# Performance work log

Hardware: AMD Instinct MI355X
Metric: run time of the kernel (lower is better)

Reference implementation:

```python
import jax, jax.numpy as jnp
import numpy as np

V, T, D, H, L, F, B = 50257, 1024, 1024, 16, 10, 4096, 2
HD = D // H  # head_dim = 64
EPS = 1e-5


def sinusoidal_pos(seq_len, d_model):
    pos = np.arange(seq_len)[:, None].astype(np.float32)
    i = np.arange(d_model // 2).astype(np.float32)
    inv = 1.0 / (10000.0 ** (2.0 * i / d_model))
    ang = pos * inv[None, :]
    pe = np.zeros((seq_len, d_model), dtype=np.float32)
    pe[:, 0::2] = np.sin(ang)
    pe[:, 1::2] = np.cos(ang)
    return jnp.asarray(pe)


def setup_inputs() -> dict:
    key = jax.random.key(0)
    ks = jax.random.split(key, 16)
    s = 0.02
    return {
        "x": jax.random.randint(ks[0], (B, T), 0, V),
        "emb": jax.random.normal(ks[1], (V, D), jnp.float32) * s,
        "pos": sinusoidal_pos(T, D),
        "Wq": jax.random.normal(ks[2], (L, D, D), jnp.float32) * s,
        "bq": jnp.zeros((L, D), jnp.float32),
        "Wk": jax.random.normal(ks[3], (L, D, D), jnp.float32) * s,
        "bk": jnp.zeros((L, D), jnp.float32),
        "Wv": jax.random.normal(ks[4], (L, D, D), jnp.float32) * s,
        "bv": jnp.zeros((L, D), jnp.float32),
        "ln_g": jnp.ones((L, D), jnp.float32),
        "ln_b": jnp.zeros((L, D), jnp.float32),
        "W1": jax.random.normal(ks[5], (L, D, F), jnp.float32) * s,
        "b1": jnp.zeros((L, F), jnp.float32),
        "W2": jax.random.normal(ks[6], (L, F, D), jnp.float32) * s,
        "b2": jnp.zeros((L, D), jnp.float32),
        "lnf_g": jnp.ones((D,), jnp.float32),
        "lnf_b": jnp.zeros((D,), jnp.float32),
        "Wout": jax.random.normal(ks[7], (D, V), jnp.float32) * s,
        "bout": jnp.zeros((V,), jnp.float32),
    }


def layer_norm(h, g, b):
    mu = jnp.mean(h, axis=-1, keepdims=True)
    var = jnp.mean(jnp.square(h - mu), axis=-1, keepdims=True)
    return (h - mu) * jax.lax.rsqrt(var + EPS) * g + b


def reference(x, emb, pos, Wq, bq, Wk, bk, Wv, bv, ln_g, ln_b, W1, b1, W2, b2, lnf_g, lnf_b, Wout, bout):
    t = x.shape[1]
    h = emb[x] + pos[None, :t]  # [B,T,D]
    causal = jnp.tril(jnp.ones((t, t), bool))  # True = keep
    scale = 1.0 / jnp.sqrt(jnp.float32(HD))

    def body(h, p):
        wq, bq_, wk, bk_, wv, bv_, g, bln, w1, b1_, w2, b2_ = p
        q = (h @ wq + bq_).reshape(B, t, H, HD)
        k = (h @ wk + bk_).reshape(B, t, H, HD)
        v = (h @ wv + bv_).reshape(B, t, H, HD)
        score = jnp.einsum('bqhd,bkhd->bhqk', q, k) * scale
        score = jnp.where(causal, score, -jnp.inf)
        attn = jax.nn.softmax(score, axis=-1)
        o = jnp.einsum('bhqk,bkhd->bqhd', attn, v).reshape(B, t, D)
        h = layer_norm(h + o, g, bln)
        m = jax.nn.gelu(h @ w1 + b1_, approximate=False) @ w2 + b2_
        h = layer_norm(h + m, g, bln)  # same LayerNorm params reused, as in source
        return h, None

    h, _ = jax.lax.scan(body, h, (Wq, bq, Wk, bk, Wv, bv, ln_g, ln_b, W1, b1, W2, b2))
    h = layer_norm(h, lnf_g, lnf_b)
    return h @ Wout + bout  # [B,T,V]
```

## Files before the change

kernel.cpp:

```cpp
#include <hip/hip_runtime.h>
#include <cstdint>
#include <cstddef>

#define Vv 50257
#define Va 50304
#define Tt 1024
#define Dd 1024
#define Hh 16
#define Ll 10
#define Ff 4096
#define Bb 2
#define Mm (Bb*Tt)
#define KSPLIT 4

typedef float f32x4 __attribute__((ext_vector_type(4)));
typedef __bf16 bf16x8 __attribute__((ext_vector_type(8)));
typedef unsigned short u16x8 __attribute__((ext_vector_type(8)));
typedef unsigned short u16x4 __attribute__((ext_vector_type(4)));

static __device__ __forceinline__ unsigned short f2bf(float f) {
  unsigned int u = __builtin_bit_cast(unsigned int, f);
  unsigned int r = (u + 0x7FFFu + ((u >> 16) & 1u)) >> 16;
  return (unsigned short)r;
}

static __device__ __forceinline__ f32x4 mfma16x16x32(u16x8 a, u16x8 b, f32x4 c) {
  return __builtin_amdgcn_mfma_f32_16x16x32_bf16(
      __builtin_bit_cast(bf16x8, a), __builtin_bit_cast(bf16x8, b), c, 0, 0, 0);
}

static __device__ __forceinline__ void async_cp16(const void* g, void* l) {
  __builtin_amdgcn_global_load_lds(
      (const __attribute__((address_space(1))) unsigned int*)g,
      (__attribute__((address_space(3))) unsigned int*)l, 16, 0, 0);
}

__global__ __launch_bounds__(256) void embed_kernel(
    const int* __restrict__ x, const float* __restrict__ emb,
    const float* __restrict__ pos, float* __restrict__ h,
    unsigned short* __restrict__ hb) {
  int bt = blockIdx.x;
  int t = bt & (Tt - 1);
  int tok = x[bt];
  int i = threadIdx.x * 4;
  f32x4 e = *(const f32x4*)(emb + (size_t)tok * Dd + i);
  f32x4 p = *(const f32x4*)(pos + (size_t)t * Dd + i);
  f32x4 r = e + p;
  *(f32x4*)(h + (size_t)bt * Dd + i) = r;
  u16x4 rb = { f2bf(r[0]), f2bf(r[1]), f2bf(r[2]), f2bf(r[3]) };
  *(u16x4*)(hb + (size_t)bt * Dd + i) = rb;
}

__global__ __launch_bounds__(256) void add_ln_kernel(
    const float* __restrict__ hin, const float* __restrict__ r,
    const float* __restrict__ g, const float* __restrict__ bb,
    float* __restrict__ hout, unsigned short* __restrict__ hbout) {
  int row = blockIdx.x;
  int tid = threadIdx.x;
  size_t off = (size_t)row * Dd + tid * 4;
  f32x4 xv = *(const f32x4*)(hin + off);
  if (r) xv += *(const f32x4*)(r + off);
  float s  = xv[0] + xv[1] + xv[2] + xv[3];
  float ss = xv[0]*xv[0] + xv[1]*xv[1] + xv[2]*xv[2] + xv[3]*xv[3];
  #pragma unroll
  for (int o = 1; o < 64; o <<= 1) {
    s  += __shfl_xor(s, o);
    ss += __shfl_xor(ss, o);
  }
  __shared__ float red[8];
  int wave = tid >> 6, lane = tid & 63;
  if (lane == 0) { red[wave] = s; red[4 + wave] = ss; }
  __syncthreads();
  s  = red[0] + red[1] + red[2] + red[3];
  ss = red[4] + red[5] + red[6] + red[7];
  float mu = s * (1.0f / Dd);
  float var = ss * (1.0f / Dd) - mu * mu;
  float rstd = rsqrtf(var + 1e-5f);
  f32x4 gv = *(const f32x4*)(g + tid * 4);
  f32x4 bv = *(const f32x4*)(bb + tid * 4);
  f32x4 y;
  #pragma unroll
  for (int j = 0; j < 4; ++j) y[j] = (xv[j] - mu) * rstd * gv[j] + bv[j];
  *(f32x4*)(hout + off) = y;
  u16x4 yb = { f2bf(y[0]), f2bf(y[1]), f2bf(y[2]), f2bf(y[3]) };
  *(u16x4*)(hbout + off) = yb;
}

__global__ __launch_bounds__(256) void add_ln_red_kernel(
    const float* __restrict__ hin, const float* __restrict__ parts,
    const float* __restrict__ bias2,
    const float* __restrict__ g, const float* __restrict__ bb,
    float* __restrict__ hout, unsigned short* __restrict__ hbout) {
  int row = blockIdx.x;
  int tid = threadIdx.x;
  size_t off = (size_t)row * Dd + tid * 4;
  f32x4 xv = *(const f32x4*)(hin + off);
  xv += *(const f32x4*)(bias2 + tid * 4);
  #pragma unroll
  for (int s = 0; s < KSPLIT; ++s)
    xv += *(const f32x4*)(parts + (size_t)s * Mm * Dd + off);
  float s  = xv[0] + xv[1] + xv[2] + xv[3];
  float ss = xv[0]*xv[0] + xv[1]*xv[1] + xv[2]*xv[2] + xv[3]*xv[3];
  #pragma unroll
  for (int o = 1; o < 64; o <<= 1) {
    s  += __shfl_xor(s, o);
    ss += __shfl_xor(ss, o);
  }
  __shared__ float red[8];
  int wave = tid >> 6, lane = tid & 63;
  if (lane == 0) { red[wave] = s; red[4 + wave] = ss; }
  __syncthreads();
  s  = red[0] + red[1] + red[2] + red[3];
  ss = red[4] + red[5] + red[6] + red[7];
  float mu = s * (1.0f / Dd);
  float var = ss * (1.0f / Dd) - mu * mu;
  float rstd = rsqrtf(var + 1e-5f);
  f32x4 gv = *(const f32x4*)(g + tid * 4);
  f32x4 bv = *(const f32x4*)(bb + tid * 4);
  f32x4 y;
  #pragma unroll
  for (int j = 0; j < 4; ++j) y[j] = (xv[j] - mu) * rstd * gv[j] + bv[j];
  *(f32x4*)(hout + off) = y;
  u16x4 yb = { f2bf(y[0]), f2bf(y[1]), f2bf(y[2]), f2bf(y[3]) };
  *(u16x4*)(hbout + off) = yb;
}

__global__ __launch_bounds__(256) void bias_gather_kernel(
    const float* __restrict__ bq, const float* __restrict__ bk,
    const float* __restrict__ bv, float* __restrict__ cb) {
  int l = blockIdx.x;
  int i = threadIdx.x * 4;
  f32x4 q = *(const f32x4*)(bq + (size_t)l * Dd + i);
  f32x4 k = *(const f32x4*)(bk + (size_t)l * Dd + i);
  f32x4 v = *(const f32x4*)(bv + (size_t)l * Dd + i);
  *(f32x4*)(cb + (size_t)l * 3072 + i) = q;
  *(f32x4*)(cb + (size_t)l * 3072 + 1024 + i) = k;
  *(f32x4*)(cb + (size_t)l * 3072 + 2048 + i) = v;
}

__global__ __launch_bounds__(256) void tconv_kernel(
    const float* __restrict__ W, unsigned short* __restrict__ Wt,
    int K, int N, int Nvalid, size_t sW, size_t sWt) {
  const float* Wl = W + (size_t)blockIdx.z * sW;
  unsigned short* Wtl = Wt + (size_t)blockIdx.z * sWt;
  __shared__ unsigned short t[64][72];
  int n0 = blockIdx.x * 64, k0 = blockIdx.y * 64;
  int tx = threadIdx.x & 15, ty = threadIdx.x >> 4;
  #pragma unroll
  for (int i = 0; i < 4; ++i) {
    int kr = ty + i * 16;
    int nc = tx * 4;
    int gn = n0 + nc;
    f32x4 v = {0.f, 0.f, 0.f, 0.f};
    if (gn + 3 < Nvalid) {
      v = *(const f32x4*)(Wl + (size_t)(k0 + kr) * N + gn);
    } else {
      #pragma unroll
      for (int j = 0; j < 4; ++j)
        if (gn + j < Nvalid) v[j] = Wl[(size_t)(k0 + kr) * N + gn + j];
    }
    t[nc + 0][kr] = f2bf(v[0]); t[nc + 1][kr] = f2bf(v[1]);
    t[nc + 2][kr] = f2bf(v[2]); t[nc + 3][kr] = f2bf(v[3]);
  }
  __syncthreads();
  #pragma unroll
  for (int i = 0; i < 4; ++i) {
    int nr = ty + i * 16;
    u16x4 o = *(const u16x4*)&t[nr][tx * 4];
    *(u16x4*)(Wtl + (size_t)(n0 + nr) * K + k0 + tx * 4) = o;
  }
}

template <int BM, int BN, int WR, int WC, int EPI, bool SWZ, int KS>
__global__ __launch_bounds__(256) void gemm_bt(
    const unsigned short* __restrict__ A, const unsigned short* __restrict__ Bt,
    const float* __restrict__ bias, void* __restrict__ Cout,
    int Ncols, int K, size_t zstr) {
  static_assert(WR * WC == 4, "4 waves");
  constexpr int MI = BM / WR / 16;
  constexpr int NJ = BN / WC / 16;
  __shared__ __align__(16) unsigned short Al[2][BM * 32];
  __shared__ __align__(16) unsigned short Bl[2][BN * 32];
  int bx = blockIdx.x, by = blockIdx.y;
  if constexpr (SWZ) {
    unsigned gx = gridDim.x;
    unsigned total = gx * gridDim.y;
    unsigned flat = by * gx + bx;
    unsigned per = total >> 3;
    unsigned work = (flat & 7u) * per + (flat >> 3);
    bx = work % gx; by = work / gx;
  }
  const int bm = bx * BM;
  const int bn = by * BN;
  const int tid = threadIdx.x, lane = tid & 63, wave = tid >> 6;
  const int wm = (wave / WC) * (BM / WR);
  const int wn = (wave % WC) * (BN / WC);
  const int rowi = lane >> 2;
  const int koff = (lane & 3) * 8;

  auto stage = [&](int buf, int k0) {
    #pragma unroll
    for (int i = 0; i < BM / 64; ++i) {
      int ch = wave + i * 4;
      async_cp16(A + (size_t)(bm + ch * 16 + rowi) * K + k0 + koff, &Al[buf][ch * 512]);
    }
    #pragma unroll
    for (int i = 0; i < BN / 64; ++i) {
      int ch = wave + i * 4;
      async_cp16(Bt + (size_t)(bn + ch * 16 + rowi) * K + k0 + koff, &Bl[buf][ch * 512]);
    }
  };

  f32x4 acc[MI][NJ];
  #pragma unroll
  for (int i = 0; i < MI; ++i)
    #pragma unroll
    for (int j = 0; j < NJ; ++j) acc[i][j] = {0.f, 0.f, 0.f, 0.f};

  const int kbeg = (KS > 1) ? (int)blockIdx.z * (K / KS) : 0;
  const int kend = kbeg + K / KS;

  stage(0, kbeg);
  __syncthreads();
  int cur = 0;
  for (int k0 = kbeg; k0 < kend; k0 += 32) {
    if (k0 + 32 < kend) stage(cur ^ 1, k0 + 32);
    u16x8 af[MI], bfr[NJ];
    #pragma unroll
    for (int i = 0; i < MI; ++i)
      af[i] = *(const u16x8*)&Al[cur][(wm + i * 16 + (lane & 15)) * 32 + (lane >> 4) * 8];
    #pragma unroll
    for (int j = 0; j < NJ; ++j)
      bfr[j] = *(const u16x8*)&Bl[cur][(wn + j * 16 + (lane & 15)) * 32 + (lane >> 4) * 8];
    #pragma unroll
    for (int i = 0; i < MI; ++i)
      #pragma unroll
      for (int j = 0; j < NJ; ++j)
        acc[i][j] = mfma16x16x32(af[i], bfr[j], acc[i][j]);
    __syncthreads();
    cur ^= 1;
  }

  float bvv[NJ];
  #pragma unroll
  for (int j = 0; j < NJ; ++j) {
    if constexpr (EPI != 3) {
      int col = bn + wn + j * 16 + (lane & 15);
      bvv[j] = (col < Ncols) ? bias[col] : 0.0f;
    } else bvv[j] = 0.0f;
  }
  float* Cz = (EPI == 3) ? ((float*)Cout + (size_t)blockIdx.z * zstr) : (float*)Cout;
  #pragma unroll
  for (int i = 0; i < MI; ++i) {
    #pragma unroll
    for (int rr = 0; rr < 4; ++rr) {
      int row = bm + wm + i * 16 + (lane >> 4) * 4 + rr;
      #pragma unroll
      for (int j = 0; j < NJ; ++j) {
        int col = bn + wn + j * 16 + (lane & 15);
        if (col < Ncols) {
          float val = acc[i][j][rr] + bvv[j];
          if constexpr (EPI == 0) {
            ((float*)Cout)[(size_t)row * Ncols + col] = val;
          } else if constexpr (EPI == 1) {
            ((unsigned short*)Cout)[(size_t)row * Ncols + col] = f2bf(val);
          } else if constexpr (EPI == 2) {
            float gv = 0.5f * val * (1.0f + erff(val * 0.70710678f));
            ((unsigned short*)Cout)[(size_t)row * Ncols + col] = f2bf(gv);
          } else {
            Cz[(size_t)row * Ncols + col] = val;
          }
        }
      }
    }
  }
}

template <int EPI>
__global__ __launch_bounds__(256) void gemm_f32b(
    const unsigned short* __restrict__ A, const float* __restrict__ Bw,
    const float* __restrict__ bias, void* __restrict__ Cout, int N, int K) {
  __shared__ __align__(16) unsigned short Al[128][40];
  __shared__ __align__(16) unsigned short Btl[128][40];
  const int bn = blockIdx.x * 128;
  const int bm = blockIdx.y * 128;
  const int tid = threadIdx.x;
  const int lane = tid & 63;
  const int wave = tid >> 6;
  const int wm = (wave >> 1) * 64;
  const int wn = (wave & 1) * 64;
  const bool nfast = ((N & 3) == 0);

  f32x4 acc[4][4];
  #pragma unroll
  for (int i = 0; i < 4; ++i)
    #pragma unroll
    for (int j = 0; j < 4; ++j) acc[i][j] = {0.f, 0.f, 0.f, 0.f};

  for (int k0 = 0; k0 < K; k0 += 32) {
    __syncthreads();
    #pragma unroll
    for (int i = 0; i < 2; ++i) {
      int c = tid + i * 256;
      int row = c >> 2, ko = (c & 3) * 8;
      u16x8 v = *(const u16x8*)(A + (size_t)(bm + row) * K + k0 + ko);
      *(u16x8*)&Al[row][ko] = v;
    }
    if (nfast) {
      #pragma unroll
      for (int i = 0; i < 4; ++i) {
        int c = tid + i * 256;
        int kr = c >> 5;
        int no = (c & 31) * 4;
        f32x4 v4 = *(const f32x4*)(Bw + (size_t)(k0 + kr) * N + bn + no);
        Btl[no + 0][kr] = f2bf(v4[0]); Btl[no + 1][kr] = f2bf(v4[1]);
        Btl[no + 2][kr] = f2bf(v4[2]); Btl[no + 3][kr] = f2bf(v4[3]);
      }
    } else {
      #pragma unroll
      for (int i = 0; i < 4; ++i) {
        int c = tid + i * 256;
        int kr = c >> 5;
        int nb = c & 31;
        #pragma unroll
        for (int j = 0; j < 4; ++j) {
          int col = nb + j * 32;
          float v = (bn + col < N) ? Bw[(size_t)(k0 + kr) * N + bn + col] : 0.0f;
          Btl[col][kr] = f2bf(v);
        }
      }
    }
    __syncthreads();
    u16x8 af[4], bfr[4];
    #pragma unroll
    for (int i = 0; i < 4; ++i)
      af[i] = *(const u16x8*)&Al[wm + i * 16 + (lane & 15)][(lane >> 4) * 8];
    #pragma unroll
    for (int j = 0; j < 4; ++j)
      bfr[j] = *(const u16x8*)&Btl[wn + j * 16 + (lane & 15)][(lane >> 4) * 8];
    #pragma unroll
    for (int i = 0; i < 4; ++i)
      #pragma unroll
      for (int j = 0; j < 4; ++j)
        acc[i][j] = mfma16x16x32(af[i], bfr[j], acc[i][j]);
  }
  #pragma unroll
  for (int j = 0; j < 4; ++j) {
    int col = bn + wn + j * 16 + (lane & 15);
    bool cok = (col < N);
    float bv = cok ? bias[col] : 0.0f;
    #pragma unroll
    for (int i = 0; i < 4; ++i) {
      #pragma unroll
      for (int rr = 0; rr < 4; ++rr) {
        int row = bm + wm + i * 16 + (lane >> 4) * 4 + rr;
        float val = acc[i][j][rr] + bv;
        if (cok) {
          if constexpr (EPI == 0) ((float*)Cout)[(size_t)row * N + col] = val;
          else if constexpr (EPI == 1) ((unsigned short*)Cout)[(size_t)row * N + col] = f2bf(val);
          else {
            float gv = 0.5f * val * (1.0f + erff(val * 0.70710678f));
            ((unsigned short*)Cout)[(size_t)row * N + col] = f2bf(gv);
          }
        }
      }
    }
  }
}

__global__ __launch_bounds__(256) void attn_kernel(
    const unsigned short* __restrict__ q, const unsigned short* __restrict__ k,
    const unsigned short* __restrict__ v, float* __restrict__ o, int ld) {
  const int ys = blockIdx.y;
  const int qt = (ys < 8) ? ys : 23 - ys;
  const int bh = blockIdx.x;
  const int b = bh >> 4, h = bh & 15;
  const size_t base = (size_t)b * Tt * ld + (size_t)h * 64;
  const int tid = threadIdx.x, lane = tid & 63, wave = tid >> 6;
  const int q0 = qt * 64 + wave * 16;

  __shared__ __align__(16) unsigned short Kl[64][72];
  __shared__ __align__(16) unsigned short Vt[64][72];
  __shared__ __align__(16) unsigned short Pl[4][16][72];

  const float SC = 0.18033688011112042f;

  u16x8 qa[2];
  {
    const unsigned short* qp = q + base + (size_t)(q0 + (lane & 15)) * ld + (lane >> 4) * 8;
    qa[0] = *(const u16x8*)qp;
    qa[1] = *(const u16x8*)(qp + 32);
  }

  f32x4 Oacc[4];
  #pragma unroll
  for (int df = 0; df < 4; ++df) Oacc[df] = {0.f, 0.f, 0.f, 0.f};
  float m_run[4], l_run[4];
  #pragma unroll
  for (int rr = 0; rr < 4; ++rr) { m_run[rr] = -__builtin_inff(); l_run[rr] = 0.f; }

  for (int kt = 0; kt <= qt; ++kt) {
    __syncthreads();
    #pragma unroll
    for (int i = 0; i < 2; ++i) {
      int c = tid + i * 256;
      int rr = c >> 3, dof = (c & 7) * 8;
      *(u16x8*)&Kl[rr][dof] =
          *(const u16x8*)(k + base + (size_t)(kt * 64 + rr) * ld + dof);
    }
    #pragma unroll
    for (int i = 0; i < 2; ++i) {
      int c = tid + i * 256;
      int rr = c >> 3, dof = (c & 7) * 8;
      u16x8 vv = *(const u16x8*)(v + base + (size_t)(kt * 64 + rr) * ld + dof);
      #pragma unroll
      for (int j = 0; j < 8; ++j) {
        int d = dof + j;
        Vt[d][(rr + (d & 56)) & 63] = vv[j];
      }
    }
    __syncthreads();

    f32x4 S[4];
    #pragma unroll
    for (int nf = 0; nf < 4; ++nf) {
      S[nf] = {0.f, 0.f, 0.f, 0.f};
      #pragma unroll
      for (int s = 0; s < 2; ++s) {
        u16x8 kb = *(const u16x8*)&Kl[nf * 16 + (lane & 15)][s * 32 + (lane >> 4) * 8];
        S[nf] = mfma16x16x32(qa[s], kb, S[nf]);
      }
    }
    const int kbase = kt * 64;
    float mx[4];
    #pragma unroll
    for (int rr = 0; rr < 4; ++rr) mx[rr] = -__builtin_inff();
    #pragma unroll
    for (int nf = 0; nf < 4; ++nf) {
      int kcol = kbase + nf * 16 + (lane & 15);
      #pragma unroll
      for (int rr = 0; rr < 4; ++rr) {
        int qrow = q0 + (lane >> 4) * 4 + rr;
        float sv = S[nf][rr] * SC;
        if (kcol > qrow) sv = -__builtin_inff();
        S[nf][rr] = sv;
        mx[rr] = fmaxf(mx[rr], sv);
      }
    }
    #pragma unroll
    for (int rr = 0; rr < 4; ++rr) {
      #pragma unroll
      for (int off = 1; off < 16; off <<= 1)
        mx[rr] = fmaxf(mx[rr], __shfl_xor(mx[rr], off));
    }
    float psum[4];
    #pragma unroll
    for (int rr = 0; rr < 4; ++rr) {
      float mnew = fmaxf(m_run[rr], mx[rr]);
      float sc = exp2f(m_run[rr] - mnew);
      l_run[rr] *= sc;
      #pragma unroll
      for (int df = 0; df < 4; ++df) Oacc[df][rr] *= sc;
      m_run[rr] = mnew;
      psum[rr] = 0.f;
    }
    #pragma unroll
    for (int nf = 0; nf < 4; ++nf) {
      #pragma unroll
      for (int rr = 0; rr < 4; ++rr) {
        float pv = exp2f(S[nf][rr] - m_run[rr]);
        S[nf][rr] = pv;
        psum[rr] += pv;
      }
    }
    #pragma unroll
    for (int rr = 0; rr < 4; ++rr) {
      #pragma unroll
      for (int off = 1; off < 16; off <<= 1) psum[rr] += __shfl_xor(psum[rr], off);
      l_run[rr] += psum[rr];
    }
    #pragma unroll
    for (int nf = 0; nf < 4; ++nf)
      #pragma unroll
      for (int rr = 0; rr < 4; ++rr)
        Pl[wave][(lane >> 4) * 4 + rr][nf * 16 + (lane & 15)] = f2bf(S[nf][rr]);
    __syncthreads();
    #pragma unroll
    for (int s = 0; s < 2; ++s) {
      u16x8 pa = *(const u16x8*)&Pl[wave][lane & 15][s * 32 + (lane >> 4) * 8];
      #pragma unroll
      for (int df = 0; df < 4; ++df) {
        int d = df * 16 + (lane & 15);
        int cs = (s * 32 + (lane >> 4) * 8 + (d & 56)) & 63;
        u16x8 vb = *(const u16x8*)&Vt[d][cs];
        Oacc[df] = mfma16x16x32(pa, vb, Oacc[df]);
      }
    }
  }

  #pragma unroll
  for (int df = 0; df < 4; ++df) {
    int d = df * 16 + (lane & 15);
    #pragma unroll
    for (int rr = 0; rr < 4; ++rr) {
      int qrow = q0 + (lane >> 4) * 4 + rr;
      o[((size_t)b * Tt + qrow) * Dd + h * 64 + d] = Oacc[df][rr] / l_run[rr];
    }
  }
}

extern "C" void kernel_launch(void* const* d_in, const int* in_sizes, int n_in,
                              void* d_out, int out_size, void* d_ws, size_t ws_size,
                              hipStream_t stream) {
  const int*   x     = (const int*)d_in[0];
  const float* emb   = (const float*)d_in[1];
  const float* pos   = (const float*)d_in[2];
  const float* Wq    = (const float*)d_in[3];
  const float* bq    = (const float*)d_in[4];
  const float* Wk    = (const float*)d_in[5];
  const float* bk    = (const float*)d_in[6];
  const float* Wv    = (const float*)d_in[7];
  const float* bv    = (const float*)d_in[8];
  const float* ln_g  = (const float*)d_in[9];
  const float* ln_b  = (const float*)d_in[10];
  const float* W1    = (const float*)d_in[11];
  const float* b1    = (const float*)d_in[12];
  const float* W2    = (const float*)d_in[13];
  const float* b2    = (const float*)d_in[14];
  const float* lnf_g = (const float*)d_in[15];
  const float* lnf_b = (const float*)d_in[16];
  const float* Wout  = (const float*)d_in[17];
  const float* bout  = (const float*)d_in[18];
  float* out = (float*)d_out;

  char* p = (char*)d_ws;
  auto alloc = [&](size_t bytes) {
    char* r = p; p += (bytes + 255) & ~(size_t)255; return r;
  };
  float* h           = (float*)alloc((size_t)Mm * Dd * 4);
  unsigned short* hb = (unsigned short*)alloc((size_t)Mm * Dd * 2);
  unsigned short* qkv = (unsigned short*)alloc((size_t)Mm * 3072 * 2);
  float* of          = (float*)alloc((size_t)Mm * Dd * 4);
  unsigned short* a1 = (unsigned short*)alloc((size_t)Mm * Ff * 2);
  float* cb          = (float*)alloc((size_t)Ll * 3072 * 4);
  float* parts       = (float*)alloc((size_t)KSPLIT * Mm * Dd * 4);
  size_t base_used = (size_t)(p - (char*)d_ws);

  const size_t SZ_WQKVT = (size_t)Ll * 3072 * Dd * 2;
  const size_t SZ_W1T   = (size_t)Ll * Ff * Dd * 2;
  const size_t SZ_W2T   = (size_t)Ll * Dd * Ff * 2;
  const size_t SZ_WOUTT = (size_t)Va * Dd * 2;
  const size_t need_big = base_used + SZ_WQKVT + SZ_W1T + SZ_W2T + SZ_WOUTT + 4096;
  const size_t need_rot = base_used + SZ_WOUTT + 4096;

  embed_kernel<<<Mm, 256, 0, stream>>>(x, emb, pos, h, hb);

  if (ws_size >= need_rot) {
    bias_gather_kernel<<<Ll, 256, 0, stream>>>(bq, bk, bv, cb);
    const bool big = (ws_size >= need_big);
    unsigned short *wqkvt, *w1t, *w2t, *woutt;
    if (big) {
      wqkvt = (unsigned short*)alloc(SZ_WQKVT);
      w1t   = (unsigned short*)alloc(SZ_W1T);
      w2t   = (unsigned short*)alloc(SZ_W2T);
      woutt = (unsigned short*)alloc(SZ_WOUTT);
      tconv_kernel<<<dim3(16, 16, Ll), 256, 0, stream>>>(
          Wq, wqkvt,           Dd, Dd, Dd, (size_t)Dd*Dd, (size_t)3072*Dd);
      tconv_kernel<<<dim3(16, 16, Ll), 256, 0, stream>>>(
          Wk, wqkvt + 1024*Dd, Dd, Dd, Dd, (size_t)Dd*Dd, (size_t)3072*Dd);
      tconv_kernel<<<dim3(16, 16, Ll), 256, 0, stream>>>(
          Wv, wqkvt + 2048*Dd, Dd, Dd, Dd, (size_t)Dd*Dd, (size_t)3072*Dd);
      tconv_kernel<<<dim3(Ff/64, Dd/64, Ll), 256, 0, stream>>>(
          W1, w1t, Dd, Ff, Ff, (size_t)Dd*Ff, (size_t)Ff*Dd);
      tconv_kernel<<<dim3(Dd/64, Ff/64, Ll), 256, 0, stream>>>(
          W2, w2t, Ff, Dd, Dd, (size_t)Ff*Dd, (size_t)Dd*Ff);
      tconv_kernel<<<dim3(Va/64, Dd/64, 1), 256, 0, stream>>>(
          Wout, woutt, Dd, Vv, Vv, 0, 0);
    } else {
      unsigned short* wbuf = (unsigned short*)alloc(SZ_WOUTT);
      wqkvt = w1t = w2t = woutt = wbuf;
    }

    for (int l = 0; l < Ll; ++l) {
      unsigned short* wq_l = big ? (wqkvt + (size_t)l * 3072 * Dd) : wqkvt;
      if (!big) {
        tconv_kernel<<<dim3(16, 16, 1), 256, 0, stream>>>(Wq + (size_t)l * Dd * Dd, wq_l,           Dd, Dd, Dd, 0, 0);
        tconv_kernel<<<dim3(16, 16, 1), 256, 0, stream>>>(Wk + (size_t)l * Dd * Dd, wq_l + 1024*Dd, Dd, Dd, Dd, 0, 0);
        tconv_kernel<<<dim3(16, 16, 1), 256, 0, stream>>>(Wv + (size_t)l * Dd * Dd, wq_l + 2048*Dd, Dd, Dd, Dd, 0, 0);
      }
      gemm_bt<128, 128, 2, 2, 1, false, 1><<<dim3(Mm/128, 3072/128), 256, 0, stream>>>(
          hb, wq_l, cb + (size_t)l * 3072, qkv, 3072, Dd, 0);
      attn_kernel<<<dim3(Bb*Hh, Tt/64), 256, 0, stream>>>(qkv, qkv + 1024, qkv + 2048, of, 3072);
      add_ln_kernel<<<Mm, 256, 0, stream>>>(h, of, ln_g + (size_t)l * Dd,
                                            ln_b + (size_t)l * Dd, h, hb);
      unsigned short* w1_l = big ? (w1t + (size_t)l * Ff * Dd) : w1t;
      if (!big)
        tconv_kernel<<<dim3(Ff/64, Dd/64, 1), 256, 0, stream>>>(W1 + (size_t)l * Dd * Ff, w1_l, Dd, Ff, Ff, 0, 0);
      gemm_bt<128, 128, 2, 2, 2, false, 1><<<dim3(Mm/128, Ff/128), 256, 0, stream>>>(
          hb, w1_l, b1 + (size_t)l * Ff, a1, Ff, Dd, 0);
      unsigned short* w2_l = big ? (w2t + (size_t)l * Dd * Ff) : w2t;
      if (!big)
        tconv_kernel<<<dim3(Dd/64, Ff/64, 1), 256, 0, stream>>>(W2 + (size_t)l * Ff * Dd, w2_l, Ff, Dd, Dd, 0, 0);
      gemm_bt<128, 128, 2, 2, 3, false, KSPLIT><<<dim3(Mm/128, Dd/128, KSPLIT), 256, 0, stream>>>(
          a1, w2_l, nullptr, parts, Dd, Ff, (size_t)Mm * Dd);
      add_ln_red_kernel<<<Mm, 256, 0, stream>>>(h, parts, b2 + (size_t)l * Dd,
                                                ln_g + (size_t)l * Dd,
                                                ln_b + (size_t)l * Dd, h, hb);
    }

    add_ln_kernel<<<Mm, 256, 0, stream>>>(h, nullptr, lnf_g, lnf_b, h, hb);
    if (!big)
      tconv_kernel<<<dim3(Va/64, Dd/64, 1), 256, 0, stream>>>(Wout, woutt, Dd, Vv, Vv, 0, 0);
    gemm_bt<128, 128, 2, 2, 0, true, 1><<<dim3(Mm/128, Va/128), 256, 0, stream>>>(
        hb, woutt, bout, out, Vv, Dd, 0);
  } else {
    unsigned short* qb = qkv;
    unsigned short* kb = qkv + (size_t)Mm * Dd;
    unsigned short* vb = qkv + (size_t)2 * Mm * Dd;
    for (int l = 0; l < Ll; ++l) {
      const size_t wo = (size_t)l * Dd * Dd;
      gemm_f32b<1><<<dim3(Dd/128, Mm/128), 256, 0, stream>>>(hb, Wq + wo, bq + (size_t)l*Dd, qb, Dd, Dd);
      gemm_f32b<1><<<dim3(Dd/128, Mm/128), 256, 0, stream>>>(hb, Wk + wo, bk + (size_t)l*Dd, kb, Dd, Dd);
      gemm_f32b<1><<<dim3(Dd/128, Mm/128), 256, 0, stream>>>(hb, Wv + wo, bv + (size_t)l*Dd, vb, Dd, Dd);
      attn_kernel<<<dim3(Bb*Hh, Tt/64), 256, 0, stream>>>(qb, kb, vb, of, Dd);
      add_ln_kernel<<<Mm, 256, 0, stream>>>(h, of, ln_g + (size_t)l*Dd, ln_b + (size_t)l*Dd, h, hb);
      gemm_f32b<2><<<dim3(Ff/128, Mm/128), 256, 0, stream>>>(hb, W1 + (size_t)l*Dd*Ff, b1 + (size_t)l*Ff, a1, Ff, Dd);
      gemm_f32b<0><<<dim3(Dd/128, Mm/128), 256, 0, stream>>>(a1, W2 + (size_t)l*Ff*Dd, b2 + (size_t)l*Dd, of, Dd, Ff);
      add_ln_kernel<<<Mm, 256, 0, stream>>>(h, of, ln_g + (size_t)l*Dd, ln_b + (size_t)l*Dd, h, hb);
    }
    add_ln_kernel<<<Mm, 256, 0, stream>>>(h, nullptr, lnf_g, lnf_b, h, hb);
    gemm_f32b<0><<<dim3((Vv + 127)/128, Mm/128), 256, 0, stream>>>(hb, Wout, bout, out, Vv, Dd);
  }
}
```

Baseline: 2.324 ms.

## Split-K the QKV GEMM with reduction kernel and XOR-swizzle GEMM LDS layout

The QKV projection GEMM now runs with split-K of 2 and writes fp32 partials to a new workspace buffer. A new reduction kernel sums the partials, adds the bias and converts to bf16. The shared GEMM template also XOR-swizzles the k-chunk placement in LDS during staging and fragment reads, to reduce bank conflicts in every GEMM. Split-K doubles the grid for better CU occupancy, at the cost of extra fp32 partial traffic (2x2048x3072 floats), an extra launch and more workspace.

```diff
diff --git a/kernel.cpp b/kernel.cpp
--- a/kernel.cpp
+++ b/kernel.cpp
@@ -12,6 +12,7 @@
 #define Bb 2
 #define Mm (Bb*Tt)
 #define KSPLIT 4
+#define QSPLIT 2
 
 typedef float f32x4 __attribute__((ext_vector_type(4)));
 typedef __bf16 bf16x8 __attribute__((ext_vector_type(8)));
@@ -123,6 +124,21 @@
   *(f32x4*)(hout + off) = y;
   u16x4 yb = { f2bf(y[0]), f2bf(y[1]), f2bf(y[2]), f2bf(y[3]) };
   *(u16x4*)(hbout + off) = yb;
+}
+
+__global__ __launch_bounds__(256) void qkv_red_kernel(
+    const float* __restrict__ qp, const float* __restrict__ cbl,
+    unsigned short* __restrict__ qkvout) {
+  int row = blockIdx.y;
+  int col = blockIdx.x * 1024 + threadIdx.x * 4;
+  size_t off = (size_t)row * 3072 + col;
+  f32x4 v = *(const f32x4*)(qp + off);
+  #pragma unroll
+  for (int s = 1; s < QSPLIT; ++s)
+    v += *(const f32x4*)(qp + (size_t)s * Mm * 3072 + off);
+  v += *(const f32x4*)(cbl + col);
+  u16x4 o = { f2bf(v[0]), f2bf(v[1]), f2bf(v[2]), f2bf(v[3]) };
+  *(u16x4*)(qkvout + off) = o;
 }
 
 __global__ __launch_bounds__(256) void bias_gather_kernel(
@@ -196,18 +212,18 @@
   const int wm = (wave / WC) * (BM / WR);
   const int wn = (wave % WC) * (BN / WC);
   const int rowi = lane >> 2;
-  const int koff = (lane & 3) * 8;
+  const int kswz = ((lane & 3) ^ ((rowi >> 1) & 3)) * 8;
 
   auto stage = [&](int buf, int k0) {
     #pragma unroll
     for (int i = 0; i < BM / 64; ++i) {
       int ch = wave + i * 4;
-      async_cp16(A + (size_t)(bm + ch * 16 + rowi) * K + k0 + koff, &Al[buf][ch * 512]);
+      async_cp16(A + (size_t)(bm + ch * 16 + rowi) * K + k0 + kswz, &Al[buf][ch * 512]);
     }
     #pragma unroll
     for (int i = 0; i < BN / 64; ++i) {
       int ch = wave + i * 4;
-      async_cp16(Bt + (size_t)(bn + ch * 16 + rowi) * K + k0 + koff, &Bl[buf][ch * 512]);
+      async_cp16(Bt + (size_t)(bn + ch * 16 + rowi) * K + k0 + kswz, &Bl[buf][ch * 512]);
     }
   };
 
@@ -227,11 +243,17 @@
     if (k0 + 32 < kend) stage(cur ^ 1, k0 + 32);
     u16x8 af[MI], bfr[NJ];
     #pragma unroll
-    for (int i = 0; i < MI; ++i)
-      af[i] = *(const u16x8*)&Al[cur][(wm + i * 16 + (lane & 15)) * 32 + (lane >> 4) * 8];
-    #pragma unroll
-    for (int j = 0; j < NJ; ++j)
-      bfr[j] = *(const u16x8*)&Bl[cur][(wn + j * 16 + (lane & 15)) * 32 + (lane >> 4) * 8];
+    for (int i = 0; i < MI; ++i) {
+      int ar = wm + i * 16 + (lane & 15);
+      int sl = (lane >> 4) ^ ((ar >> 1) & 3);
+      af[i] = *(const u16x8*)&Al[cur][ar * 32 + sl * 8];
+    }
+    #pragma unroll
+    for (int j = 0; j < NJ; ++j) {
+      int br = wn + j * 16 + (lane & 15);
+      int sl = (lane >> 4) ^ ((br >> 1) & 3);
+      bfr[j] = *(const u16x8*)&Bl[cur][br * 32 + sl * 8];
+    }
     #pragma unroll
     for (int i = 0; i < MI; ++i)
       #pragma unroll
@@ -544,6 +566,7 @@
   unsigned short* a1 = (unsigned short*)alloc((size_t)Mm * Ff * 2);
   float* cb          = (float*)alloc((size_t)Ll * 3072 * 4);
   float* parts       = (float*)alloc((size_t)KSPLIT * Mm * Dd * 4);
+  float* qparts      = (float*)alloc((size_t)QSPLIT * Mm * 3072 * 4);
   size_t base_used = (size_t)(p - (char*)d_ws);
 
   const size_t SZ_WQKVT = (size_t)Ll * 3072 * Dd * 2;
@@ -588,8 +611,9 @@
         tconv_kernel<<<dim3(16, 16, 1), 256, 0, stream>>>(Wk + (size_t)l * Dd * Dd, wq_l + 1024*Dd, Dd, Dd, Dd, 0, 0);
         tconv_kernel<<<dim3(16, 16, 1), 256, 0, stream>>>(Wv + (size_t)l * Dd * Dd, wq_l + 2048*Dd, Dd, Dd, Dd, 0, 0);
       }
-      gemm_bt<128, 128, 2, 2, 1, false, 1><<<dim3(Mm/128, 3072/128), 256, 0, stream>>>(
-          hb, wq_l, cb + (size_t)l * 3072, qkv, 3072, Dd, 0);
+      gemm_bt<128, 128, 2, 2, 3, false, QSPLIT><<<dim3(Mm/128, 3072/128, QSPLIT), 256, 0, stream>>>(
+          hb, wq_l, nullptr, qparts, 3072, Dd, (size_t)Mm * 3072);
+      qkv_red_kernel<<<dim3(3, Mm), 256, 0, stream>>>(qparts, cb + (size_t)l * 3072, qkv);
       attn_kernel<<<dim3(Bb*Hh, Tt/64), 256, 0, stream>>>(qkv, qkv + 1024, qkv + 2048, of, 3072);
       add_ln_kernel<<<Mm, 256, 0, stream>>>(h, of, ln_g + (size_t)l * Dd,
                                             ln_b + (size_t)l * Dd, h, hb);
```

After: 2.265 ms, median of 2. 2.5% less time.
